# Optimization experiments

Hardware: AMD Instinct MI355X
Metric: run time of the kernel (lower is better)

## Reference

```python
import jax, jax.numpy as jnp
import numpy as np

DIM = 256
NUM_HEADS = 8
WH, WW = 7, 7
N = WH * WW
HEAD_DIM = DIM // NUM_HEADS
SCALE = HEAD_DIM ** -0.5
B_ = 4096
NW = 64  # windows per image


def _relative_position_index():
    # Swin relative position index: (N, N) int32 in [0, (2Wh-1)*(2Ww-1))
    coords = np.stack(np.meshgrid(np.arange(WH), np.arange(WW), indexing='ij'))  # (2, Wh, Ww)
    cf = coords.reshape(2, -1)  # (2, N)
    rel = cf[:, :, None] - cf[:, None, :]  # (2, N, N)
    rel = rel.transpose(1, 2, 0).copy()
    rel[:, :, 0] += WH - 1
    rel[:, :, 1] += WW - 1
    rel[:, :, 0] *= 2 * WW - 1
    return jnp.asarray(rel.sum(-1), dtype=jnp.int32)  # (N, N)


def setup_inputs() -> dict:
    key = jax.random.key(0)
    ks = jax.random.split(key, 7)
    x = jax.random.normal(ks[0], (B_, N, DIM), dtype=jnp.float32)
    mask = jax.random.normal(ks[1], (NW, N, N), dtype=jnp.float32)
    qkv_w = jax.random.normal(ks[2], (3 * DIM, DIM), dtype=jnp.float32) * 0.02
    qkv_b = jnp.zeros((3 * DIM,), dtype=jnp.float32)
    proj_w = jax.random.normal(ks[3], (DIM, DIM), dtype=jnp.float32) * 0.02
    proj_b = jnp.zeros((DIM,), dtype=jnp.float32)
    bias_table = jax.random.normal(ks[4], ((2 * WH - 1) * (2 * WW - 1), NUM_HEADS), dtype=jnp.float32) * 0.02
    rel_index = _relative_position_index()
    return {"x": x, "mask": mask, "qkv_w": qkv_w, "qkv_b": qkv_b,
            "proj_w": proj_w, "proj_b": proj_b, "bias_table": bias_table,
            "rel_index": rel_index}


def reference(x, mask, qkv_w, qkv_b, proj_w, proj_b, bias_table, rel_index):
    Bw, n, c = x.shape
    # qkv projection: (B_, N, 3C) -> (3, B_, nH, N, hd)
    qkv = (x @ qkv_w.T + qkv_b).reshape(Bw, n, 3, NUM_HEADS, HEAD_DIM)
    qkv = qkv.transpose(2, 0, 3, 1, 4)
    q, k, v = qkv[0], qkv[1], qkv[2]
    attn = jnp.einsum('bhqd,bhkd->bhqk', q * SCALE, k)  # (B_, nH, N, N)
    # gathered relative position bias: (nH, N, N)
    rpb = bias_table[rel_index.reshape(-1)].reshape(n, n, NUM_HEADS).transpose(2, 0, 1)
    attn = attn + rpb[None]
    # window mask: reshape batch into (B, nW) and broadcast mask per-window
    nW = mask.shape[0]
    attn = attn.reshape(Bw // nW, nW, NUM_HEADS, n, n) + mask[None, :, None]
    attn = attn.reshape(Bw, NUM_HEADS, n, n)
    attn = jax.nn.softmax(attn, axis=-1)
    out = jnp.einsum('bhqk,bhkd->bhqd', attn, v)  # (B_, nH, N, hd)
    out = out.transpose(0, 2, 1, 3).reshape(Bw, n, c)
    return out @ proj_w.T + proj_b
```

## Files before the change

kernel.cpp:

```cpp
#include <hip/hip_runtime.h>
#include <hip/hip_bf16.h>

typedef __bf16 bf16;
typedef __bf16 bf16x8 __attribute__((ext_vector_type(8)));
typedef float  f32x4  __attribute__((ext_vector_type(4)));

#define MFMA16(A,B,C) __builtin_amdgcn_mfma_f32_16x16x32_bf16((A),(B),(C),0,0,0)

constexpr float SCALE = 0.17677669529663687f;

constexpr size_t CB_OFF    = 0;
constexpr size_t QKVW_OFF  = 8388608;
constexpr size_t PROJW_OFF = QKVW_OFF + 768*256*2;
constexpr size_t QI_OFF    = PROJW_OFF + 256*256*2;
constexpr size_t TEN_ELEMS = 51380224ull;
constexpr size_t AO_OFF    = QI_OFF + 3*TEN_ELEMS*2;

__global__ __launch_bounds__(256) void build_cb_kernel(
    const float* __restrict__ bias_table, const float* __restrict__ mask,
    const int* __restrict__ rel_index, float* __restrict__ cb) {
  int idx = blockIdx.x * 256 + threadIdx.x;
  int j = idx & 63, m = (idx >> 6) & 63, h = (idx >> 12) & 7, w = idx >> 15;
  float v = 0.f;
  if (j < 49 && m < 49)
    v = bias_table[rel_index[m * 49 + j] * 8 + h] + mask[(w * 49 + m) * 49 + j];
  cb[idx] = v;
}

__global__ __launch_bounds__(256) void cvt_w_kernel(
    const float* __restrict__ qkv_w, const float* __restrict__ proj_w,
    bf16* __restrict__ qkv_wb, bf16* __restrict__ proj_wb) {
  int i = blockIdx.x * 256 + threadIdx.x;
  if (i < 768 * 256) qkv_wb[i] = (bf16)qkv_w[i];
  else               proj_wb[i - 768 * 256] = (bf16)proj_w[i - 768 * 256];
}

__device__ __forceinline__ bf16x8 frag(const bf16* S, int row, int kchunk) {
  return *reinterpret_cast<const bf16x8*>(&S[row * 64 + ((kchunk ^ (row & 7)) * 8)]);
}

__global__ __launch_bounds__(256) void gemm_qkv_kernel(
    const float* __restrict__ x, const bf16* __restrict__ qkv_wb,
    const float* __restrict__ qkv_b, bf16* __restrict__ qkv_i) {
  __shared__ __align__(16) bf16 As[128 * 64];
  __shared__ __align__(16) bf16 Bs[128 * 64];
  const int bid = blockIdx.x;
  const int xcd = bid & 7, idx = bid >> 3;
  const int m_t = xcd * 196 + idx / 6;
  const int n_t = idx % 6;
  const int tid = threadIdx.x;
  const int wv = tid >> 6, l = tid & 63, l15 = l & 15, lgp = l >> 4;
  const int wr = wv >> 1, wc = wv & 1;

  const f32x4 fzero = {0.f, 0.f, 0.f, 0.f};
  f32x4 acc[4][4];
#pragma unroll
  for (int mt = 0; mt < 4; ++mt)
#pragma unroll
    for (int nt = 0; nt < 4; ++nt) acc[mt][nt] = fzero;

  for (int ks = 0; ks < 4; ++ks) {
    const int k0 = ks * 64;
#pragma unroll
    for (int i = 0; i < 4; ++i) {
      int c = i * 256 + tid;
      int row = c >> 3, kc = c & 7;
      const float* src = x + (size_t)(m_t * 128 + row) * 256 + k0 + kc * 8;
      f32x4 f0 = *reinterpret_cast<const f32x4*>(src);
      f32x4 f1 = *reinterpret_cast<const f32x4*>(src + 4);
      bf16x8 v8;
#pragma unroll
      for (int e = 0; e < 4; ++e) { v8[e] = (bf16)f0[e]; v8[e + 4] = (bf16)f1[e]; }
      *reinterpret_cast<bf16x8*>(&As[row * 64 + ((kc ^ (row & 7)) * 8)]) = v8;
    }
#pragma unroll
    for (int i = 0; i < 4; ++i) {
      int c = i * 256 + tid;
      int row = c >> 3, kc = c & 7;
      bf16x8 w8 = *reinterpret_cast<const bf16x8*>(
          qkv_wb + (size_t)(n_t * 128 + row) * 256 + k0 + kc * 8);
      *reinterpret_cast<bf16x8*>(&Bs[row * 64 + ((kc ^ (row & 7)) * 8)]) = w8;
    }
    __syncthreads();
#pragma unroll
    for (int kk = 0; kk < 2; ++kk) {
      bf16x8 Af[4], Bf[4];
#pragma unroll
      for (int mt = 0; mt < 4; ++mt) Af[mt] = frag(As, wr * 64 + mt * 16 + l15, kk * 4 + lgp);
#pragma unroll
      for (int nt = 0; nt < 4; ++nt) Bf[nt] = frag(Bs, wc * 64 + nt * 16 + l15, kk * 4 + lgp);
#pragma unroll
      for (int mt = 0; mt < 4; ++mt)
#pragma unroll
        for (int nt = 0; nt < 4; ++nt) acc[mt][nt] = MFMA16(Af[mt], Bf[nt], acc[mt][nt]);
    }
    __syncthreads();
  }

  const int tsel = n_t >> 1;
  bf16* tb = qkv_i + (size_t)tsel * TEN_ELEMS;
  const float sc = (tsel == 0) ? SCALE : 1.0f;
  float bias[4]; int hh[4], dd[4];
#pragma unroll
  for (int nt = 0; nt < 4; ++nt) {
    int n_g = n_t * 128 + wc * 64 + nt * 16 + l15;
    bias[nt] = qkv_b[n_g];
    int nl = n_g & 255;
    hh[nt] = nl >> 5; dd[nt] = nl & 31;
  }
#pragma unroll
  for (int mt = 0; mt < 4; ++mt) {
#pragma unroll
    for (int r = 0; r < 4; ++r) {
      int r_g = m_t * 128 + wr * 64 + mt * 16 + lgp * 4 + r;
      int b = r_g / 49, m = r_g - b * 49;
#pragma unroll
      for (int nt = 0; nt < 4; ++nt) {
        tb[((size_t)(b * 8 + hh[nt]) * 49 + m) * 32 + dd[nt]] =
            (bf16)((acc[mt][nt][r] + bias[nt]) * sc);
      }
    }
  }
}

__device__ __forceinline__ bf16x8 repack8(f32x4 Ta, f32x4 Tb, int l15, int lgp) {
  const int s0 = l15 + ((lgp & 1) << 5);
  const bool hi = (lgp & 2) != 0;
  bf16x8 F;
#pragma unroll
  for (int r = 0; r < 4; ++r) {
    float a0 = __shfl(Ta[r], s0);
    float b0 = __shfl(Tb[r], s0);
    F[r] = (bf16)(hi ? b0 : a0);
    float a1 = __shfl(Ta[r], s0 + 16);
    float b1 = __shfl(Tb[r], s0 + 16);
    F[r + 4] = (bf16)(hi ? b1 : a1);
  }
  return F;
}

__global__ __launch_bounds__(256) void attn_kernel(
    const bf16* __restrict__ qkv_i, const float* __restrict__ cb,
    bf16* __restrict__ ao) {
  __shared__ __align__(16) bf16 Vs[4][64 * 32];
  const int tid = threadIdx.x, wv = tid >> 6, l = tid & 63;
  const int l15 = l & 15, lgp = l >> 4;
  const int g = blockIdx.x * 4 + wv;
  const int b = g >> 3, h = g & 7;

  const bf16* qp = qkv_i + (size_t)(b * 8 + h) * 1568;
  const bf16* kp = qp + TEN_ELEMS;
  const bf16* vp = kp + TEN_ELEMS;
  bf16* vsm = &Vs[wv][0];

#pragma unroll
  for (int i = 0; i < 4; ++i) {
    int c = i * 64 + l;
    if (c < 196)
      *reinterpret_cast<bf16x8*>(&vsm[c * 8]) =
          *reinterpret_cast<const bf16x8*>(vp + c * 8);
  }
  {
    const bf16x8 z8 = {(bf16)0.f,(bf16)0.f,(bf16)0.f,(bf16)0.f,
                       (bf16)0.f,(bf16)0.f,(bf16)0.f,(bf16)0.f};
    if (l < 60) *reinterpret_cast<bf16x8*>(&vsm[1568 + l * 8]) = z8;
  }
  __syncthreads();

  bf16x8 Qf[4], Kf[4];
#pragma unroll
  for (int mt = 0; mt < 4; ++mt) {
    int m = mt * 16 + l15; int mc = m < 49 ? m : 48;
    Qf[mt] = *reinterpret_cast<const bf16x8*>(qp + mc * 32 + lgp * 8);
  }
#pragma unroll
  for (int jt = 0; jt < 4; ++jt) {
    int j = jt * 16 + l15; int jc = j < 49 ? j : 48;
    Kf[jt] = *reinterpret_cast<const bf16x8*>(kp + jc * 32 + lgp * 8);
  }
  bf16x8 Vb[2][2];
#pragma unroll
  for (int dt = 0; dt < 2; ++dt)
#pragma unroll
    for (int ksx = 0; ksx < 2; ++ksx) {
#pragma unroll
      for (int u = 0; u < 8; ++u) {
        int j = ksx * 32 + lgp * 8 + u;
        Vb[dt][ksx][u] = vsm[j * 32 + dt * 16 + l15];
      }
    }

  const float* cbp = cb + (size_t)((b & 63) * 8 + h) * 4096;
  bf16* aob = ao + (size_t)b * 12544;
  const f32x4 fzero = {0.f, 0.f, 0.f, 0.f};

#pragma unroll
  for (int mt = 0; mt < 4; ++mt) {
    int mrow = mt * 16 + l15;
    f32x4 e4[4];
#pragma unroll
    for (int jt = 0; jt < 4; ++jt) e4[jt] = MFMA16(Kf[jt], Qf[mt], fzero);
#pragma unroll
    for (int jt = 0; jt < 4; ++jt) {
      f32x4 c4 = *reinterpret_cast<const f32x4*>(cbp + mrow * 64 + jt * 16 + lgp * 4);
#pragma unroll
      for (int r = 0; r < 4; ++r) e4[jt][r] += c4[r];
    }
    if (lgp != 0) { e4[3][0] = -3.0e38f; }
    e4[3][1] = -3.0e38f; e4[3][2] = -3.0e38f; e4[3][3] = -3.0e38f;

    float mx = e4[0][0];
#pragma unroll
    for (int jt = 0; jt < 4; ++jt)
#pragma unroll
      for (int r = 0; r < 4; ++r) mx = fmaxf(mx, e4[jt][r]);
    mx = fmaxf(mx, __shfl_xor(mx, 16));
    mx = fmaxf(mx, __shfl_xor(mx, 32));
    float sum = 0.f;
#pragma unroll
    for (int jt = 0; jt < 4; ++jt)
#pragma unroll
      for (int r = 0; r < 4; ++r) {
        float ex = __expf(e4[jt][r] - mx);
        e4[jt][r] = ex;
        sum += ex;
      }
    sum += __shfl_xor(sum, 16);
    sum += __shfl_xor(sum, 32);
    float rinv = 1.0f / sum;
#pragma unroll
    for (int jt = 0; jt < 4; ++jt)
#pragma unroll
      for (int r = 0; r < 4; ++r) e4[jt][r] *= rinv;

    bf16x8 Pf0 = repack8(e4[0], e4[1], l15, lgp);
    bf16x8 Pf1 = repack8(e4[2], e4[3], l15, lgp);
    f32x4 pv[2];
#pragma unroll
    for (int dt = 0; dt < 2; ++dt) {
      pv[dt] = MFMA16(Pf0, Vb[dt][0], fzero);
      pv[dt] = MFMA16(Pf1, Vb[dt][1], pv[dt]);
    }
#pragma unroll
    for (int r = 0; r < 4; ++r) {
      int m_g = mt * 16 + lgp * 4 + r;
      if (m_g < 49) {
#pragma unroll
        for (int dt = 0; dt < 2; ++dt)
          aob[m_g * 256 + h * 32 + dt * 16 + l15] = (bf16)pv[dt][r];
      }
    }
  }
}

__global__ __launch_bounds__(256) void gemm_proj_kernel(
    const bf16* __restrict__ ao, const bf16* __restrict__ proj_wb,
    const float* __restrict__ proj_b, float* __restrict__ out) {
  __shared__ __align__(16) bf16 As[128 * 64];
  __shared__ __align__(16) bf16 Bs[128 * 64];
  const int bid = blockIdx.x;
  const int xcd = bid & 7, idx = bid >> 3;
  const int m_t = xcd * 196 + idx / 2;
  const int n_t = idx % 2;
  const int tid = threadIdx.x;
  const int wv = tid >> 6, l = tid & 63, l15 = l & 15, lgp = l >> 4;
  const int wr = wv >> 1, wc = wv & 1;

  const f32x4 fzero = {0.f, 0.f, 0.f, 0.f};
  f32x4 acc[4][4];
#pragma unroll
  for (int mt = 0; mt < 4; ++mt)
#pragma unroll
    for (int nt = 0; nt < 4; ++nt) acc[mt][nt] = fzero;

  for (int ks = 0; ks < 4; ++ks) {
    const int k0 = ks * 64;
#pragma unroll
    for (int i = 0; i < 4; ++i) {
      int c = i * 256 + tid;
      int row = c >> 3, kc = c & 7;
      bf16x8 a8 = *reinterpret_cast<const bf16x8*>(
          ao + (size_t)(m_t * 128 + row) * 256 + k0 + kc * 8);
      *reinterpret_cast<bf16x8*>(&As[row * 64 + ((kc ^ (row & 7)) * 8)]) = a8;
      bf16x8 w8 = *reinterpret_cast<const bf16x8*>(
          proj_wb + (size_t)(n_t * 128 + row) * 256 + k0 + kc * 8);
      *reinterpret_cast<bf16x8*>(&Bs[row * 64 + ((kc ^ (row & 7)) * 8)]) = w8;
    }
    __syncthreads();
#pragma unroll
    for (int kk = 0; kk < 2; ++kk) {
      bf16x8 Af[4], Bf[4];
#pragma unroll
      for (int mt = 0; mt < 4; ++mt) Af[mt] = frag(As, wr * 64 + mt * 16 + l15, kk * 4 + lgp);
#pragma unroll
      for (int nt = 0; nt < 4; ++nt) Bf[nt] = frag(Bs, wc * 64 + nt * 16 + l15, kk * 4 + lgp);
#pragma unroll
      for (int mt = 0; mt < 4; ++mt)
#pragma unroll
        for (int nt = 0; nt < 4; ++nt) acc[mt][nt] = MFMA16(Af[mt], Bf[nt], acc[mt][nt]);
    }
    __syncthreads();
  }

  float bias[4]; int cg[4];
#pragma unroll
  for (int nt = 0; nt < 4; ++nt) {
    cg[nt] = n_t * 128 + wc * 64 + nt * 16 + l15;
    bias[nt] = proj_b[cg[nt]];
  }
#pragma unroll
  for (int mt = 0; mt < 4; ++mt) {
#pragma unroll
    for (int r = 0; r < 4; ++r) {
      size_t r_g = (size_t)(m_t * 128 + wr * 64 + mt * 16 + lgp * 4 + r);
#pragma unroll
      for (int nt = 0; nt < 4; ++nt)
        out[r_g * 256 + cg[nt]] = acc[mt][nt][r] + bias[nt];
    }
  }
}

extern "C" void kernel_launch(void* const* d_in, const int* in_sizes, int n_in,
                              void* d_out, int out_size, void* d_ws, size_t ws_size,
                              hipStream_t stream) {
  const float* x          = (const float*)d_in[0];
  const float* mask       = (const float*)d_in[1];
  const float* qkv_w      = (const float*)d_in[2];
  const float* qkv_b      = (const float*)d_in[3];
  const float* proj_w     = (const float*)d_in[4];
  const float* proj_b     = (const float*)d_in[5];
  const float* bias_table = (const float*)d_in[6];
  const int*   rel_index  = (const int*)d_in[7];

  char* ws = (char*)d_ws;
  float* cb      = (float*)(ws + CB_OFF);
  bf16*  qkv_wb  = (bf16*)(ws + QKVW_OFF);
  bf16*  proj_wb = (bf16*)(ws + PROJW_OFF);
  bf16*  qkv_i   = (bf16*)(ws + QI_OFF);
  bf16*  ao      = (bf16*)(ws + AO_OFF);

  hipLaunchKernelGGL(build_cb_kernel, dim3(8192), dim3(256), 0, stream,
                     bias_table, mask, rel_index, cb);
  hipLaunchKernelGGL(cvt_w_kernel, dim3(1024), dim3(256), 0, stream,
                     qkv_w, proj_w, qkv_wb, proj_wb);
  hipLaunchKernelGGL(gemm_qkv_kernel, dim3(9408), dim3(256), 0, stream,
                     x, qkv_wb, qkv_b, qkv_i);
  hipLaunchKernelGGL(attn_kernel, dim3(8192), dim3(256), 0, stream,
                     qkv_i, cb, ao);
  hipLaunchKernelGGL(gemm_proj_kernel, dim3(3136), dim3(256), 0, stream,
                     ao, proj_wb, proj_b, (float*)d_out);
}
```

Before: 435.4 us.

## Restructure QKV GEMM to full-N row tiles with register-prefetched x and direct weight loads

The QKV GEMM now gives each 512-thread block a 64-row slab of x and all 768 output columns, so x is read and converted to bf16 only once, where before it was reloaded for each of six column tiles. Weight fragments are read straight from global memory (expected to hit L2/L1) rather than staged through shared memory. The next x K-slice is prefetched into registers while the MFMAs run. The trade-offs are heavier per-wave register use (24 accumulators), uncoalesced global weight loads inside the inner loop, and fewer blocks.

```diff
diff --git a/kernel.cpp b/kernel.cpp
--- a/kernel.cpp
+++ b/kernel.cpp
@@ -39,72 +39,67 @@
   return *reinterpret_cast<const bf16x8*>(&S[row * 64 + ((kchunk ^ (row & 7)) * 8)]);
 }
 
-__global__ __launch_bounds__(256) void gemm_qkv_kernel(
+__global__ __launch_bounds__(512, 2) void gemm_qkv_kernel(
     const float* __restrict__ x, const bf16* __restrict__ qkv_wb,
     const float* __restrict__ qkv_b, bf16* __restrict__ qkv_i) {
-  __shared__ __align__(16) bf16 As[128 * 64];
-  __shared__ __align__(16) bf16 Bs[128 * 64];
+  __shared__ __align__(16) bf16 As[64 * 64];
   const int bid = blockIdx.x;
   const int xcd = bid & 7, idx = bid >> 3;
-  const int m_t = xcd * 196 + idx / 6;
-  const int n_t = idx % 6;
+  const int m_t = xcd * 392 + idx;
   const int tid = threadIdx.x;
   const int wv = tid >> 6, l = tid & 63, l15 = l & 15, lgp = l >> 4;
-  const int wr = wv >> 1, wc = wv & 1;
+
+  const int srow = tid >> 3, skc = tid & 7;
+  const float* sg = x + (size_t)(m_t * 64 + srow) * 256 + skc * 8;
 
   const f32x4 fzero = {0.f, 0.f, 0.f, 0.f};
-  f32x4 acc[4][4];
+  f32x4 acc[4][6];
 #pragma unroll
   for (int mt = 0; mt < 4; ++mt)
 #pragma unroll
-    for (int nt = 0; nt < 4; ++nt) acc[mt][nt] = fzero;
-
+    for (int nt = 0; nt < 6; ++nt) acc[mt][nt] = fzero;
+
+  f32x4 s0 = *reinterpret_cast<const f32x4*>(sg);
+  f32x4 s1 = *reinterpret_cast<const f32x4*>(sg + 4);
+
+#pragma unroll
   for (int ks = 0; ks < 4; ++ks) {
-    const int k0 = ks * 64;
-#pragma unroll
-    for (int i = 0; i < 4; ++i) {
-      int c = i * 256 + tid;
-      int row = c >> 3, kc = c & 7;
-      const float* src = x + (size_t)(m_t * 128 + row) * 256 + k0 + kc * 8;
-      f32x4 f0 = *reinterpret_cast<const f32x4*>(src);
-      f32x4 f1 = *reinterpret_cast<const f32x4*>(src + 4);
+    {
       bf16x8 v8;
 #pragma unroll
-      for (int e = 0; e < 4; ++e) { v8[e] = (bf16)f0[e]; v8[e + 4] = (bf16)f1[e]; }
-      *reinterpret_cast<bf16x8*>(&As[row * 64 + ((kc ^ (row & 7)) * 8)]) = v8;
-    }
-#pragma unroll
-    for (int i = 0; i < 4; ++i) {
-      int c = i * 256 + tid;
-      int row = c >> 3, kc = c & 7;
-      bf16x8 w8 = *reinterpret_cast<const bf16x8*>(
-          qkv_wb + (size_t)(n_t * 128 + row) * 256 + k0 + kc * 8);
-      *reinterpret_cast<bf16x8*>(&Bs[row * 64 + ((kc ^ (row & 7)) * 8)]) = w8;
+      for (int e = 0; e < 4; ++e) { v8[e] = (bf16)s0[e]; v8[e + 4] = (bf16)s1[e]; }
+      *reinterpret_cast<bf16x8*>(&As[srow * 64 + ((skc ^ (srow & 7)) * 8)]) = v8;
     }
     __syncthreads();
+    if (ks < 3) {
+      s0 = *reinterpret_cast<const f32x4*>(sg + (ks + 1) * 64);
+      s1 = *reinterpret_cast<const f32x4*>(sg + (ks + 1) * 64 + 4);
+    }
 #pragma unroll
     for (int kk = 0; kk < 2; ++kk) {
-      bf16x8 Af[4], Bf[4];
-#pragma unroll
-      for (int mt = 0; mt < 4; ++mt) Af[mt] = frag(As, wr * 64 + mt * 16 + l15, kk * 4 + lgp);
-#pragma unroll
-      for (int nt = 0; nt < 4; ++nt) Bf[nt] = frag(Bs, wc * 64 + nt * 16 + l15, kk * 4 + lgp);
+      bf16x8 Af[4], Bf[6];
+#pragma unroll
+      for (int mt = 0; mt < 4; ++mt) Af[mt] = frag(As, mt * 16 + l15, kk * 4 + lgp);
+#pragma unroll
+      for (int nt = 0; nt < 6; ++nt) {
+        int n_row = wv * 96 + nt * 16 + l15;
+        Bf[nt] = *reinterpret_cast<const bf16x8*>(
+            qkv_wb + (size_t)n_row * 256 + ks * 64 + kk * 32 + lgp * 8);
+      }
 #pragma unroll
       for (int mt = 0; mt < 4; ++mt)
 #pragma unroll
-        for (int nt = 0; nt < 4; ++nt) acc[mt][nt] = MFMA16(Af[mt], Bf[nt], acc[mt][nt]);
+        for (int nt = 0; nt < 6; ++nt) acc[mt][nt] = MFMA16(Af[mt], Bf[nt], acc[mt][nt]);
     }
     __syncthreads();
   }
 
-  const int tsel = n_t >> 1;
-  bf16* tb = qkv_i + (size_t)tsel * TEN_ELEMS;
-  const float sc = (tsel == 0) ? SCALE : 1.0f;
-  float bias[4]; int hh[4], dd[4];
-#pragma unroll
-  for (int nt = 0; nt < 4; ++nt) {
-    int n_g = n_t * 128 + wc * 64 + nt * 16 + l15;
+  float bias[6]; int hh[6], dd[6], ts[6];
+#pragma unroll
+  for (int nt = 0; nt < 6; ++nt) {
+    int n_g = wv * 96 + nt * 16 + l15;
     bias[nt] = qkv_b[n_g];
+    ts[nt] = n_g >> 8;
     int nl = n_g & 255;
     hh[nt] = nl >> 5; dd[nt] = nl & 31;
   }
@@ -112,11 +107,13 @@
   for (int mt = 0; mt < 4; ++mt) {
 #pragma unroll
     for (int r = 0; r < 4; ++r) {
-      int r_g = m_t * 128 + wr * 64 + mt * 16 + lgp * 4 + r;
+      int r_g = m_t * 64 + mt * 16 + lgp * 4 + r;
       int b = r_g / 49, m = r_g - b * 49;
 #pragma unroll
-      for (int nt = 0; nt < 4; ++nt) {
-        tb[((size_t)(b * 8 + hh[nt]) * 49 + m) * 32 + dd[nt]] =
+      for (int nt = 0; nt < 6; ++nt) {
+        float sc = (ts[nt] == 0) ? SCALE : 1.0f;
+        qkv_i[(size_t)ts[nt] * TEN_ELEMS +
+              ((size_t)(b * 8 + hh[nt]) * 49 + m) * 32 + dd[nt]] =
             (bf16)((acc[mt][nt][r] + bias[nt]) * sc);
       }
     }
@@ -343,7 +340,7 @@
                      bias_table, mask, rel_index, cb);
   hipLaunchKernelGGL(cvt_w_kernel, dim3(1024), dim3(256), 0, stream,
                      qkv_w, proj_w, qkv_wb, proj_wb);
-  hipLaunchKernelGGL(gemm_qkv_kernel, dim3(9408), dim3(256), 0, stream,
+  hipLaunchKernelGGL(gemm_qkv_kernel, dim3(3136), dim3(512), 0, stream,
                      x, qkv_wb, qkv_b, qkv_i);
   hipLaunchKernelGGL(attn_kernel, dim3(8192), dim3(256), 0, stream,
                      qkv_i, cb, ao);
```

Result: slower. 475.0 us (+9.1%).
